# Optimization experiments

Hardware: AMD Instinct MI355X
Metric: run time of the kernel (lower is better)

The kernel has to match this reference:

```python
import jax, jax.numpy as jnp
import numpy as np

N, DEG, FIN, HID, OUT = 50000, 16, 128, 128, 64


def setup_inputs() -> dict:
    key = jax.random.key(0)
    ks = jax.random.split(key, 32)
    x = jax.random.normal(ks[0], (N, FIN), dtype=jnp.float32)
    src = jax.random.randint(ks[1], (N * DEG,), 0, N, dtype=jnp.int32)
    dst = jnp.repeat(jnp.arange(N, dtype=jnp.int32), DEG)  # sorted by target, fixed degree
    edge_index = jnp.stack([src, dst])  # [2, E]
    dims = [(FIN, HID), (HID, HID), (HID, OUT)]
    params = {}
    i = 2
    for l, (fi, fo) in enumerate(dims, 1):
        s_lstm = 1.0 / np.sqrt(fi)
        params[f"W_ih{l}"] = jax.random.normal(ks[i + 0], (4 * fi, fi)) * s_lstm
        params[f"W_hh{l}"] = jax.random.normal(ks[i + 1], (4 * fi, fi)) * s_lstm
        params[f"b_ih{l}"] = jax.random.normal(ks[i + 2], (4 * fi,)) * s_lstm
        params[f"b_hh{l}"] = jax.random.normal(ks[i + 3], (4 * fi,)) * s_lstm
        params[f"Wl{l}"] = jax.random.normal(ks[i + 4], (fo, fi)) * (1.0 / np.sqrt(fi))
        params[f"bl{l}"] = jnp.zeros((fo,), jnp.float32)
        params[f"Wr{l}"] = jax.random.normal(ks[i + 5], (fo, fi)) * (1.0 / np.sqrt(fi))
        i += 6
    return {"x": x, "edge_index": edge_index, **params}


def _lstm_last(neigh, Wih, Whh, bih, bhh):
    # neigh: [N, deg, Fi]; PyTorch LSTM gate order i,f,g,o; return last-step output h.
    h0 = jnp.zeros((neigh.shape[0], Wih.shape[0] // 4), neigh.dtype)
    bias = bih + bhh

    def step(carry, xt):
        h, c = carry
        g = xt @ Wih.T + h @ Whh.T + bias
        i, f, gg, o = jnp.split(g, 4, axis=-1)
        c = jax.nn.sigmoid(f) * c + jax.nn.sigmoid(i) * jnp.tanh(gg)
        h = jax.nn.sigmoid(o) * jnp.tanh(c)
        return (h, c), None

    (h, _), _ = jax.lax.scan(step, (h0, h0), jnp.swapaxes(neigh, 0, 1))
    return h


def _sage_layer(x, src2d, Wih, Whh, bih, bhh, Wl, bl, Wr):
    neigh = x[src2d]  # gather: [N, deg, Fi]
    aggr = _lstm_last(neigh, Wih, Whh, bih, bhh)  # [N, Fi]
    return aggr @ Wl.T + bl + x @ Wr.T  # lin_l(aggr) + lin_r(x)


def reference(x, edge_index,
              W_ih1, W_hh1, b_ih1, b_hh1, Wl1, bl1, Wr1,
              W_ih2, W_hh2, b_ih2, b_hh2, Wl2, bl2, Wr2,
              W_ih3, W_hh3, b_ih3, b_hh3, Wl3, bl3, Wr3):
    n = x.shape[0]
    src2d = edge_index[0].reshape(n, -1)  # fixed-degree, dst-sorted edge list
    h = _sage_layer(x, src2d, W_ih1, W_hh1, b_ih1, b_hh1, Wl1, bl1, Wr1)
    h = jax.nn.relu(h)  # dropout is identity in eval mode
    h = _sage_layer(h, src2d, W_ih2, W_hh2, b_ih2, b_hh2, Wl2, bl2, Wr2)
    h = jax.nn.relu(h)
    return _sage_layer(h, src2d, W_ih3, W_hh3, b_ih3, b_hh3, Wl3, bl3, Wr3)
```

## Files before the change

### kernel.cpp

```cpp
#include <hip/hip_runtime.h>
#include <cstddef>
#include <cstdint>

typedef __attribute__((ext_vector_type(4))) float f32x4;
typedef __attribute__((ext_vector_type(8))) short short8;

#define HID 128
#define NK1 -1.4426950408889634f
#define PK2 2.8853900817779268f

#define BAR_LGKM() __asm__ volatile("s_waitcnt lgkmcnt(0)\ns_barrier" ::: "memory")
#define STEP_BAR3() __asm__ volatile("s_waitcnt vmcnt(4) lgkmcnt(0)\ns_barrier" ::: "memory")

__device__ __forceinline__ short f2bf(float f) {
  unsigned u = __builtin_bit_cast(unsigned, f);
  u += 0x7FFFu + ((u >> 16) & 1u);
  return (short)(u >> 16);
}
__device__ __forceinline__ unsigned pack_bf2(float a, float b) {
  unsigned ua = __builtin_bit_cast(unsigned, a) + 0x8000u;
  unsigned ub = __builtin_bit_cast(unsigned, b) + 0x8000u;
  return __builtin_amdgcn_perm(ub, ua, 0x07060302u);
}
__device__ __forceinline__ float2 unpack2v(int w) {
  float2 r;
  r.x = __builtin_bit_cast(float, (unsigned)(w << 16));
  r.y = __builtin_bit_cast(float, (unsigned)w & 0xffff0000u);
  return r;
}

__device__ __forceinline__ float lstm_elem(float si, float sf, float sg, float so, float& c) {
  float Ei = __builtin_amdgcn_exp2f(si);
  float Ef = __builtin_amdgcn_exp2f(sf);
  float Tg = __builtin_amdgcn_exp2f(sg);
  float Eo = __builtin_amdgcn_exp2f(so);
  float u = 1.0f + Ei, w = 1.0f + Ef, v = Tg + 1.0f, Tm = Tg - 1.0f;
  float t0 = u * v;
  float num = __builtin_fmaf(c, t0, w * Tm);
  float cn = num * __builtin_amdgcn_rcpf(w * t0);
  c = cn;
  float Tc = __builtin_amdgcn_exp2f(PK2 * cn);
  return (Tc - 1.0f) * __builtin_amdgcn_rcpf((1.0f + Eo) * (Tc + 1.0f));
}

__global__ void conv_x_kernel(const float* __restrict__ x, short* __restrict__ xb, int n,
                              int* __restrict__ tctr) {
  int i = blockIdx.x * blockDim.x + threadIdx.x;
  if (i < 8) tctr[i] = 0;
  int stride = gridDim.x * blockDim.x;
  for (; i < n; i += stride) xb[i] = f2bf(x[i]);
}

__global__ void conv_layer_kernel(const float* __restrict__ Wih, const float* __restrict__ Whh,
                                  const float* __restrict__ bih, const float* __restrict__ bhh,
                                  const float* __restrict__ Wl, const float* __restrict__ Wr, int foK,
                                  short* __restrict__ wihB, short* __restrict__ whhB,
                                  short* __restrict__ wlB, short* __restrict__ wrB,
                                  float* __restrict__ bsum) {
  int i = blockIdx.x * blockDim.x + threadIdx.x;
  if (i < 512 * HID) {
    float sc = ((i >> 14) == 2) ? PK2 : NK1;
    wihB[i] = f2bf(Wih[i] * sc);
    whhB[i] = f2bf(Whh[i] * sc);
  }
  if (i < foK) { wlB[i] = f2bf(Wl[i]); wrB[i] = f2bf(Wr[i]); }
  if (i < 512) bsum[i] = (bih[i] + bhh[i]) * (((i >> 7) == 2) ? PK2 : NK1);
}

#define OSTR 524
__global__ __launch_bounds__(512, 4) void pgemm_kernel(
    const short* __restrict__ A, const short* __restrict__ W,
    const float* __restrict__ bias, short* __restrict__ out, int M, int ntiles) {
  __shared__ short ldsO[32 * OSTR];
  const int tid = threadIdx.x;
  const int wave = tid >> 6, lane = tid & 63;
  const int quad = lane >> 4, nn = lane & 15;
  const int cbase = wave * 64;

  short8 wreg[4][4];
#pragma unroll
  for (int kt = 0; kt < 4; ++kt)
#pragma unroll
    for (int nt = 0; nt < 4; ++nt)
      wreg[kt][nt] = *(const short8*)(W + (size_t)(cbase + nt * 16 + nn) * HID + kt * 32 + quad * 8);
  f32x4 bias4[4];
#pragma unroll
  for (int nt = 0; nt < 4; ++nt)
#pragma unroll
    for (int r = 0; r < 4; ++r) bias4[nt][r] = bias[cbase + nt * 16 + quad * 4 + r];

#pragma unroll 1
  for (int rt = blockIdx.x; rt < ntiles; rt += gridDim.x) {
    const int row0 = rt * 32;
    f32x4 acc[2][4];
#pragma unroll
    for (int b = 0; b < 2; ++b)
#pragma unroll
      for (int nt = 0; nt < 4; ++nt) acc[b][nt] = bias4[nt];
#pragma unroll
    for (int kt = 0; kt < 4; ++kt) {
      int r0 = row0 + nn;      if (r0 > M - 1) r0 = M - 1;
      int r1 = row0 + 16 + nn; if (r1 > M - 1) r1 = M - 1;
      short8 af0 = *(const short8*)(A + (size_t)r0 * HID + kt * 32 + quad * 8);
      short8 af1 = *(const short8*)(A + (size_t)r1 * HID + kt * 32 + quad * 8);
#pragma unroll
      for (int nt = 0; nt < 4; ++nt) {
        acc[0][nt] = __builtin_amdgcn_mfma_f32_16x16x32_bf16(wreg[kt][nt], af0, acc[0][nt], 0, 0, 0);
        acc[1][nt] = __builtin_amdgcn_mfma_f32_16x16x32_bf16(wreg[kt][nt], af1, acc[1][nt], 0, 0, 0);
      }
    }
    BAR_LGKM();
#pragma unroll
    for (int b = 0; b < 2; ++b)
#pragma unroll
      for (int nt = 0; nt < 4; ++nt) {
        uint2 pk;
        pk.x = pack_bf2(acc[b][nt][0], acc[b][nt][1]);
        pk.y = pack_bf2(acc[b][nt][2], acc[b][nt][3]);
        *(uint2*)(ldsO + (b * 16 + nn) * OSTR + cbase + nt * 16 + quad * 4) = pk;
      }
    BAR_LGKM();
#pragma unroll
    for (int idx = tid; idx < 32 * 64; idx += 512) {
      int row = idx >> 6, c8 = (idx & 63) * 8;
      if (row0 + row < M)
        *(short8*)(out + (size_t)(row0 + row) * 512 + c8) = *(const short8*)(ldsO + row * OSTR + c8);
    }
  }
}

#define NPB 16
#define PSTR 520
#define HSTR 152
#define LSTM_LDS_BYTES ((4 * NPB * PSTR + 2 * NPB * HSTR) * 2 + 256 * 4 + 16)

template <int FO, bool RELU, bool OUTF32>
__global__ __launch_bounds__(512, 4) void lstm_fused_kernel(
    const short* __restrict__ P, const short* __restrict__ Whh,
    const int* __restrict__ src, const short* __restrict__ cur,
    const short* __restrict__ Wl, const short* __restrict__ Wr,
    const float* __restrict__ bl,
    short* __restrict__ outB, float* __restrict__ outF, int M, int ntiles,
    int* __restrict__ tctr) {
  extern __shared__ char smem[];
  short* Pb = (short*)smem;
  short* Hb = Pb + 4 * NPB * PSTR;
  int* srcL = (int*)(Hb + 2 * NPB * HSTR);
  int* nextTp = srcL + 256;

  const int tid = threadIdx.x;
  const int wave = tid >> 6, lane = tid & 63;
  const int quad = lane >> 4, nn = lane & 15;
  const int r0row = wave * 2, r1row = wave * 2 + 1;

  short8 wreg[4][4];
#pragma unroll
  for (int kt = 0; kt < 4; ++kt)
#pragma unroll
    for (int q = 0; q < 4; ++q)
      wreg[kt][q] = *(const short8*)(Whh + (size_t)(q * 128 + wave * 16 + nn) * HID + kt * 32 + quad * 8);

  f32x4 biasO = {0.f, 0.f, 0.f, 0.f};
  short8 wlR[4], wrR[4];
  if (FO == 128 || wave < 4) {
#pragma unroll
    for (int r = 0; r < 4; ++r) biasO[r] = bl[wave * 16 + quad * 4 + r];
#pragma unroll
    for (int kt = 0; kt < 4; ++kt) {
      wlR[kt] = *(const short8*)(Wl + (size_t)(wave * 16 + nn) * HID + kt * 32 + quad * 8);
      wrR[kt] = *(const short8*)(Wr + (size_t)(wave * 16 + nn) * HID + kt * 32 + quad * 8);
    }
  }

  int tile = blockIdx.x;
  while (tile < ntiles) {
    const int nodeBase = tile * NPB;
    if (tid < 256) {
      int node = nodeBase + (tid >> 4);
      srcL[tid] = (node < M) ? src[nodeBase * 16 + tid] : 0;
    }
    if (tid == 0) *nextTp = (int)gridDim.x + atomicAdd(tctr, 1);
    float c_st[4] = {0.f, 0.f, 0.f, 0.f};
    BAR_LGKM();
    const int my_next = *nextTp;

#pragma unroll
    for (int tt = 0; tt < 3; ++tt) {
      int sa = srcL[r0row * 16 + tt], sb = srcL[r1row * 16 + tt];
      __builtin_amdgcn_global_load_lds(
          (const __attribute__((address_space(1))) unsigned int*)(P + (size_t)sa * 512 + lane * 8),
          (__attribute__((address_space(3))) unsigned int*)(Pb + tt * NPB * PSTR + r0row * PSTR), 16, 0, 0);
      __builtin_amdgcn_global_load_lds(
          (const __attribute__((address_space(1))) unsigned int*)(P + (size_t)sb * 512 + lane * 8),
          (__attribute__((address_space(3))) unsigned int*)(Pb + tt * NPB * PSTR + r1row * PSTR), 16, 0, 0);
    }
    int sA = srcL[r0row * 16 + 3], sB = srcL[r1row * 16 + 3];

    int pc = 0, pg = 3;
#pragma unroll 1
    for (int t = 0; t < 16; ++t) {
      short* Pc = Pb + pc * NPB * PSTR;
      short* Pg = Pb + pg * NPB * PSTR;
      const short* Hp = Hb + ((t + 1) & 1) * NPB * HSTR;
      short* Hw = Hb + (t & 1) * NPB * HSTR;
      pc = (pc + 1) & 3;
      pg = (pg + 1) & 3;

      STEP_BAR3();

      const short* pR = Pc + nn * PSTR + wave * 16 + quad * 4;
      uint2 p0 = *(const uint2*)(pR + 0 * 128);
      uint2 p1 = *(const uint2*)(pR + 1 * 128);
      uint2 p2 = *(const uint2*)(pR + 2 * 128);
      uint2 p3 = *(const uint2*)(pR + 3 * 128);
      f32x4 acc[4];
      {
        float2 u, v;
        u = unpack2v(p0.x); v = unpack2v(p0.y);
        acc[0][0] = u.x; acc[0][1] = u.y; acc[0][2] = v.x; acc[0][3] = v.y;
        u = unpack2v(p1.x); v = unpack2v(p1.y);
        acc[1][0] = u.x; acc[1][1] = u.y; acc[1][2] = v.x; acc[1][3] = v.y;
        u = unpack2v(p2.x); v = unpack2v(p2.y);
        acc[2][0] = u.x; acc[2][1] = u.y; acc[2][2] = v.x; acc[2][3] = v.y;
        u = unpack2v(p3.x); v = unpack2v(p3.y);
        acc[3][0] = u.x; acc[3][1] = u.y; acc[3][2] = v.x; acc[3][3] = v.y;
      }

      __builtin_amdgcn_global_load_lds(
          (const __attribute__((address_space(1))) unsigned int*)(P + (size_t)sA * 512 + lane * 8),
          (__attribute__((address_space(3))) unsigned int*)(Pg + r0row * PSTR), 16, 0, 0);
      __builtin_amdgcn_global_load_lds(
          (const __attribute__((address_space(1))) unsigned int*)(P + (size_t)sB * 512 + lane * 8),
          (__attribute__((address_space(3))) unsigned int*)(Pg + r1row * PSTR), 16, 0, 0);
      {
        int tn = (t + 4 < 16) ? t + 4 : 15;
        sA = srcL[r0row * 16 + tn];
        sB = srcL[r1row * 16 + tn];
      }

      if (t) {
#pragma unroll
        for (int kt = 0; kt < 4; ++kt) {
          short8 hb = *(const short8*)(Hp + nn * HSTR + kt * 32 + quad * 8);
#pragma unroll
          for (int q = 0; q < 4; ++q)
            acc[q] = __builtin_amdgcn_mfma_f32_16x16x32_bf16(wreg[kt][q], hb, acc[q], 0, 0, 0);
        }
      }

      float hv[4];
#pragma unroll
      for (int r = 0; r < 4; ++r)
        hv[r] = lstm_elem(acc[0][r], acc[1][r], acc[2][r], acc[3][r], c_st[r]);
      uint2 pk;
      pk.x = pack_bf2(hv[0], hv[1]);
      pk.y = pack_bf2(hv[2], hv[3]);
      *(uint2*)(Hw + nn * HSTR + wave * 16 + quad * 4) = pk;
    }

    BAR_LGKM();

    if (FO == 128 || wave < 4) {
      const short* Hf = Hb + NPB * HSTR;
      const int cbase = wave * 16;
      f32x4 accO = biasO;
#pragma unroll
      for (int kt = 0; kt < 4; ++kt) {
        short8 hb = *(const short8*)(Hf + nn * HSTR + kt * 32 + quad * 8);
        accO = __builtin_amdgcn_mfma_f32_16x16x32_bf16(wlR[kt], hb, accO, 0, 0, 0);
        short8 cb = *(const short8*)(cur + (size_t)(nodeBase + nn) * HID + kt * 32 + quad * 8);
        accO = __builtin_amdgcn_mfma_f32_16x16x32_bf16(wrR[kt], cb, accO, 0, 0, 0);
      }
      if (RELU) {
#pragma unroll
        for (int r = 0; r < 4; ++r) accO[r] = fmaxf(accO[r], 0.0f);
      }
      int node = nodeBase + nn;
      if (node < M) {
        if (OUTF32) {
          *(f32x4*)(outF + (size_t)node * FO + cbase + quad * 4) = accO;
        } else {
          uint2 pko;
          pko.x = pack_bf2(accO[0], accO[1]);
          pko.y = pack_bf2(accO[2], accO[3]);
          *(uint2*)(outB + (size_t)node * FO + cbase + quad * 4) = pko;
        }
      }
    }
    tile = my_next;
  }
}

extern "C" void kernel_launch(void* const* d_in, const int* in_sizes, int n_in,
                              void* d_out, int out_size, void* d_ws, size_t ws_size,
                              hipStream_t stream) {
  const float* x = (const float*)d_in[0];
  const int* src = (const int*)d_in[1];
  const float* Wih[3] = {(const float*)d_in[2], (const float*)d_in[9], (const float*)d_in[16]};
  const float* Whh[3] = {(const float*)d_in[3], (const float*)d_in[10], (const float*)d_in[17]};
  const float* bih[3] = {(const float*)d_in[4], (const float*)d_in[11], (const float*)d_in[18]};
  const float* bhh[3] = {(const float*)d_in[5], (const float*)d_in[12], (const float*)d_in[19]};
  const float* Wl[3]  = {(const float*)d_in[6], (const float*)d_in[13], (const float*)d_in[20]};
  const float* bl[3]  = {(const float*)d_in[7], (const float*)d_in[14], (const float*)d_in[21]};
  const float* Wr[3]  = {(const float*)d_in[8], (const float*)d_in[15], (const float*)d_in[22]};

  const int M = in_sizes[0] / HID;

  char* ws = (char*)d_ws;
  size_t off = 0;
  auto alloc = [&](size_t bytes) -> void* {
    void* p = ws + off;
    off += (bytes + 255) & ~(size_t)255;
    return p;
  };
  short* curA = (short*)alloc((size_t)M * HID * 2);
  short* curB = (short*)alloc((size_t)M * HID * 2);
  short* Pbuf = (short*)alloc((size_t)M * 512 * 2);
  short* wihB[3]; short* whhB[3]; short* wlB[3]; short* wrB[3]; float* bsum[3];
  for (int l = 0; l < 3; ++l) {
    wihB[l] = (short*)alloc(512 * HID * 2);
    whhB[l] = (short*)alloc(512 * HID * 2);
    wlB[l]  = (short*)alloc(HID * HID * 2);
    wrB[l]  = (short*)alloc(HID * HID * 2);
    bsum[l] = (float*)alloc(512 * 4);
  }
  int* tctr = (int*)alloc(256);

  const int nltiles = (M + NPB - 1) / NPB;
  const int ntiles = (M + 31) / 32;

  (void)hipFuncSetAttribute((const void*)lstm_fused_kernel<128, true, false>,
                            hipFuncAttributeMaxDynamicSharedMemorySize, LSTM_LDS_BYTES);
  (void)hipFuncSetAttribute((const void*)lstm_fused_kernel<64, false, true>,
                            hipFuncAttributeMaxDynamicSharedMemorySize, LSTM_LDS_BYTES);

  conv_x_kernel<<<2048, 256, 0, stream>>>(x, curA, M * HID, tctr);
  for (int l = 0; l < 3; ++l) {
    const int Fo = (l == 2) ? 64 : 128;
    conv_layer_kernel<<<256, 256, 0, stream>>>(Wih[l], Whh[l], bih[l], bhh[l], Wl[l], Wr[l],
                                               Fo * HID, wihB[l], whhB[l], wlB[l], wrB[l], bsum[l]);
  }

  short* cur = curA;
  short* nxt = curB;
  for (int l = 0; l < 3; ++l) {
    pgemm_kernel<<<784, 512, 0, stream>>>(cur, wihB[l], bsum[l], Pbuf, M, ntiles);
    if (l < 2) {
      lstm_fused_kernel<128, true, false><<<512, 512, LSTM_LDS_BYTES, stream>>>(
          Pbuf, whhB[l], src, cur, wlB[l], wrB[l], bl[l], nxt, nullptr, M, nltiles, tctr + l);
      short* tswap = cur; cur = nxt; nxt = tswap;
    } else {
      lstm_fused_kernel<64, false, true><<<512, 512, LSTM_LDS_BYTES, stream>>>(
          Pbuf, whhB[l], src, cur, wlB[l], wrB[l], bl[l], nullptr, (float*)d_out, M, nltiles, tctr + 2);
    }
  }
}
```

Measured before the change: 787.2 us.

## Process 32 nodes per LSTM tile with triple-buffered neighbor prefetch

Doubles the node tile of the fused LSTM kernel from 16 to 32, so each wave issues two MFMA chains against the same register-resident W_hh fragments. That gives more independent work per weight load and per barrier. The P prefetch ring shrinks from four buffers to three, which shortens the lookahead from three steps to two. Launch bounds and grid size are halved to match. The larger LDS footprint likely limits residency to one block per CU. The epilogue is rebalanced so that all eight waves take part in the 64-wide output layer.

```diff
diff --git a/kernel.cpp b/kernel.cpp
--- a/kernel.cpp
+++ b/kernel.cpp
@@ -10,7 +10,7 @@
 #define PK2 2.8853900817779268f
 
 #define BAR_LGKM() __asm__ volatile("s_waitcnt lgkmcnt(0)\ns_barrier" ::: "memory")
-#define STEP_BAR3() __asm__ volatile("s_waitcnt vmcnt(4) lgkmcnt(0)\ns_barrier" ::: "memory")
+#define STEP_BAR() __asm__ volatile("s_waitcnt vmcnt(4) lgkmcnt(0)\ns_barrier" ::: "memory")
 
 __device__ __forceinline__ short f2bf(float f) {
   unsigned u = __builtin_bit_cast(unsigned, f);
@@ -129,13 +129,14 @@
   }
 }
 
-#define NPB 16
+#define NPB 32
 #define PSTR 520
 #define HSTR 152
-#define LSTM_LDS_BYTES ((4 * NPB * PSTR + 2 * NPB * HSTR) * 2 + 256 * 4 + 16)
+#define NPBUF 3
+#define LSTM_LDS_BYTES ((NPBUF * NPB * PSTR + 2 * NPB * HSTR) * 2 + 512 * 4 + 16)
 
 template <int FO, bool RELU, bool OUTF32>
-__global__ __launch_bounds__(512, 4) void lstm_fused_kernel(
+__global__ __launch_bounds__(512, 2) void lstm_fused_kernel(
     const short* __restrict__ P, const short* __restrict__ Whh,
     const int* __restrict__ src, const short* __restrict__ cur,
     const short* __restrict__ Wl, const short* __restrict__ Wr,
@@ -144,14 +145,14 @@
     int* __restrict__ tctr) {
   extern __shared__ char smem[];
   short* Pb = (short*)smem;
-  short* Hb = Pb + 4 * NPB * PSTR;
+  short* Hb = Pb + NPBUF * NPB * PSTR;
   int* srcL = (int*)(Hb + 2 * NPB * HSTR);
-  int* nextTp = srcL + 256;
+  int* nextTp = srcL + 512;
 
   const int tid = threadIdx.x;
   const int wave = tid >> 6, lane = tid & 63;
   const int quad = lane >> 4, nn = lane & 15;
-  const int r0row = wave * 2, r1row = wave * 2 + 1;
+  const int grow = wave * 4;
 
   short8 wreg[4][4];
 #pragma unroll
@@ -160,131 +161,178 @@
     for (int q = 0; q < 4; ++q)
       wreg[kt][q] = *(const short8*)(Whh + (size_t)(q * 128 + wave * 16 + nn) * HID + kt * 32 + quad * 8);
 
-  f32x4 biasO = {0.f, 0.f, 0.f, 0.f};
+  const int ecol = (FO == 128) ? wave * 16 : (wave & 3) * 16;
+  f32x4 biasO;
   short8 wlR[4], wrR[4];
-  if (FO == 128 || wave < 4) {
-#pragma unroll
-    for (int r = 0; r < 4; ++r) biasO[r] = bl[wave * 16 + quad * 4 + r];
-#pragma unroll
-    for (int kt = 0; kt < 4; ++kt) {
-      wlR[kt] = *(const short8*)(Wl + (size_t)(wave * 16 + nn) * HID + kt * 32 + quad * 8);
-      wrR[kt] = *(const short8*)(Wr + (size_t)(wave * 16 + nn) * HID + kt * 32 + quad * 8);
-    }
+#pragma unroll
+  for (int r = 0; r < 4; ++r) biasO[r] = bl[ecol + quad * 4 + r];
+#pragma unroll
+  for (int kt = 0; kt < 4; ++kt) {
+    wlR[kt] = *(const short8*)(Wl + (size_t)(ecol + nn) * HID + kt * 32 + quad * 8);
+    wrR[kt] = *(const short8*)(Wr + (size_t)(ecol + nn) * HID + kt * 32 + quad * 8);
   }
 
   int tile = blockIdx.x;
   while (tile < ntiles) {
     const int nodeBase = tile * NPB;
-    if (tid < 256) {
+    {
       int node = nodeBase + (tid >> 4);
       srcL[tid] = (node < M) ? src[nodeBase * 16 + tid] : 0;
     }
     if (tid == 0) *nextTp = (int)gridDim.x + atomicAdd(tctr, 1);
-    float c_st[4] = {0.f, 0.f, 0.f, 0.f};
+    float c0[4] = {0.f, 0.f, 0.f, 0.f};
+    float c1[4] = {0.f, 0.f, 0.f, 0.f};
     BAR_LGKM();
     const int my_next = *nextTp;
 
 #pragma unroll
-    for (int tt = 0; tt < 3; ++tt) {
-      int sa = srcL[r0row * 16 + tt], sb = srcL[r1row * 16 + tt];
-      __builtin_amdgcn_global_load_lds(
-          (const __attribute__((address_space(1))) unsigned int*)(P + (size_t)sa * 512 + lane * 8),
-          (__attribute__((address_space(3))) unsigned int*)(Pb + tt * NPB * PSTR + r0row * PSTR), 16, 0, 0);
-      __builtin_amdgcn_global_load_lds(
-          (const __attribute__((address_space(1))) unsigned int*)(P + (size_t)sb * 512 + lane * 8),
-          (__attribute__((address_space(3))) unsigned int*)(Pb + tt * NPB * PSTR + r1row * PSTR), 16, 0, 0);
-    }
-    int sA = srcL[r0row * 16 + 3], sB = srcL[r1row * 16 + 3];
-
-    int pc = 0, pg = 3;
+    for (int tt = 0; tt < 2; ++tt) {
+#pragma unroll
+      for (int j = 0; j < 4; ++j) {
+        int s = srcL[(grow + j) * 16 + tt];
+        __builtin_amdgcn_global_load_lds(
+            (const __attribute__((address_space(1))) unsigned int*)(P + (size_t)s * 512 + lane * 8),
+            (__attribute__((address_space(3))) unsigned int*)(Pb + tt * NPB * PSTR + (grow + j) * PSTR),
+            16, 0, 0);
+      }
+    }
+
+    int pc = 0, pg = 2;
 #pragma unroll 1
     for (int t = 0; t < 16; ++t) {
       short* Pc = Pb + pc * NPB * PSTR;
       short* Pg = Pb + pg * NPB * PSTR;
       const short* Hp = Hb + ((t + 1) & 1) * NPB * HSTR;
       short* Hw = Hb + (t & 1) * NPB * HSTR;
-      pc = (pc + 1) & 3;
-      pg = (pg + 1) & 3;
-
-      STEP_BAR3();
-
-      const short* pR = Pc + nn * PSTR + wave * 16 + quad * 4;
-      uint2 p0 = *(const uint2*)(pR + 0 * 128);
-      uint2 p1 = *(const uint2*)(pR + 1 * 128);
-      uint2 p2 = *(const uint2*)(pR + 2 * 128);
-      uint2 p3 = *(const uint2*)(pR + 3 * 128);
-      f32x4 acc[4];
+      pc = (pc == NPBUF - 1) ? 0 : pc + 1;
+      pg = (pg == NPBUF - 1) ? 0 : pg + 1;
+
+      STEP_BAR();
+
+      f32x4 acc0[4], acc1[4];
       {
+        const short* pR = Pc + nn * PSTR + wave * 16 + quad * 4;
+        uint2 q0 = *(const uint2*)(pR + 0 * 128);
+        uint2 q1 = *(const uint2*)(pR + 1 * 128);
+        uint2 q2 = *(const uint2*)(pR + 2 * 128);
+        uint2 q3 = *(const uint2*)(pR + 3 * 128);
         float2 u, v;
-        u = unpack2v(p0.x); v = unpack2v(p0.y);
-        acc[0][0] = u.x; acc[0][1] = u.y; acc[0][2] = v.x; acc[0][3] = v.y;
-        u = unpack2v(p1.x); v = unpack2v(p1.y);
-        acc[1][0] = u.x; acc[1][1] = u.y; acc[1][2] = v.x; acc[1][3] = v.y;
-        u = unpack2v(p2.x); v = unpack2v(p2.y);
-        acc[2][0] = u.x; acc[2][1] = u.y; acc[2][2] = v.x; acc[2][3] = v.y;
-        u = unpack2v(p3.x); v = unpack2v(p3.y);
-        acc[3][0] = u.x; acc[3][1] = u.y; acc[3][2] = v.x; acc[3][3] = v.y;
-      }
-
-      __builtin_amdgcn_global_load_lds(
-          (const __attribute__((address_space(1))) unsigned int*)(P + (size_t)sA * 512 + lane * 8),
-          (__attribute__((address_space(3))) unsigned int*)(Pg + r0row * PSTR), 16, 0, 0);
-      __builtin_amdgcn_global_load_lds(
-          (const __attribute__((address_space(1))) unsigned int*)(P + (size_t)sB * 512 + lane * 8),
-          (__attribute__((address_space(3))) unsigned int*)(Pg + r1row * PSTR), 16, 0, 0);
+        u = unpack2v(q0.x); v = unpack2v(q0.y);
+        acc0[0][0] = u.x; acc0[0][1] = u.y; acc0[0][2] = v.x; acc0[0][3] = v.y;
+        u = unpack2v(q1.x); v = unpack2v(q1.y);
+        acc0[1][0] = u.x; acc0[1][1] = u.y; acc0[1][2] = v.x; acc0[1][3] = v.y;
+        u = unpack2v(q2.x); v = unpack2v(q2.y);
+        acc0[2][0] = u.x; acc0[2][1] = u.y; acc0[2][2] = v.x; acc0[2][3] = v.y;
+        u = unpack2v(q3.x); v = unpack2v(q3.y);
+        acc0[3][0] = u.x; acc0[3][1] = u.y; acc0[3][2] = v.x; acc0[3][3] = v.y;
+      }
       {
-        int tn = (t + 4 < 16) ? t + 4 : 15;
-        sA = srcL[r0row * 16 + tn];
-        sB = srcL[r1row * 16 + tn];
+        const short* pR = Pc + (16 + nn) * PSTR + wave * 16 + quad * 4;
+        uint2 q0 = *(const uint2*)(pR + 0 * 128);
+        uint2 q1 = *(const uint2*)(pR + 1 * 128);
+        uint2 q2 = *(const uint2*)(pR + 2 * 128);
+        uint2 q3 = *(const uint2*)(pR + 3 * 128);
+        float2 u, v;
+        u = unpack2v(q0.x); v = unpack2v(q0.y);
+        acc1[0][0] = u.x; acc1[0][1] = u.y; acc1[0][2] = v.x; acc1[0][3] = v.y;
+        u = unpack2v(q1.x); v = unpack2v(q1.y);
+        acc1[1][0] = u.x; acc1[1][1] = u.y; acc1[1][2] = v.x; acc1[1][3] = v.y;
+        u = unpack2v(q2.x); v = unpack2v(q2.y);
+        acc1[2][0] = u.x; acc1[2][1] = u.y; acc1[2][2] = v.x; acc1[2][3] = v.y;
+        u = unpack2v(q3.x); v = unpack2v(q3.y);
+        acc1[3][0] = u.x; acc1[3][1] = u.y; acc1[3][2] = v.x; acc1[3][3] = v.y;
+      }
+
+      {
+        int tn = (t + 2 < 16) ? t + 2 : 15;
+#pragma unroll
+        for (int j = 0; j < 4; ++j) {
+          int s = srcL[(grow + j) * 16 + tn];
+          __builtin_amdgcn_global_load_lds(
+              (const __attribute__((address_space(1))) unsigned int*)(P + (size_t)s * 512 + lane * 8),
+              (__attribute__((address_space(3))) unsigned int*)(Pg + (grow + j) * PSTR), 16, 0, 0);
+        }
       }
 
       if (t) {
 #pragma unroll
         for (int kt = 0; kt < 4; ++kt) {
-          short8 hb = *(const short8*)(Hp + nn * HSTR + kt * 32 + quad * 8);
-#pragma unroll
-          for (int q = 0; q < 4; ++q)
-            acc[q] = __builtin_amdgcn_mfma_f32_16x16x32_bf16(wreg[kt][q], hb, acc[q], 0, 0, 0);
-        }
-      }
-
-      float hv[4];
+          short8 hb0 = *(const short8*)(Hp + nn * HSTR + kt * 32 + quad * 8);
+          short8 hb1 = *(const short8*)(Hp + (16 + nn) * HSTR + kt * 32 + quad * 8);
+#pragma unroll
+          for (int q = 0; q < 4; ++q) {
+            acc0[q] = __builtin_amdgcn_mfma_f32_16x16x32_bf16(wreg[kt][q], hb0, acc0[q], 0, 0, 0);
+            acc1[q] = __builtin_amdgcn_mfma_f32_16x16x32_bf16(wreg[kt][q], hb1, acc1[q], 0, 0, 0);
+          }
+        }
+      }
+
+      float hv0[4], hv1[4];
 #pragma unroll
       for (int r = 0; r < 4; ++r)
-        hv[r] = lstm_elem(acc[0][r], acc[1][r], acc[2][r], acc[3][r], c_st[r]);
-      uint2 pk;
-      pk.x = pack_bf2(hv[0], hv[1]);
-      pk.y = pack_bf2(hv[2], hv[3]);
-      *(uint2*)(Hw + nn * HSTR + wave * 16 + quad * 4) = pk;
+        hv0[r] = lstm_elem(acc0[0][r], acc0[1][r], acc0[2][r], acc0[3][r], c0[r]);
+#pragma unroll
+      for (int r = 0; r < 4; ++r)
+        hv1[r] = lstm_elem(acc1[0][r], acc1[1][r], acc1[2][r], acc1[3][r], c1[r]);
+      uint2 pk0, pk1;
+      pk0.x = pack_bf2(hv0[0], hv0[1]);
+      pk0.y = pack_bf2(hv0[2], hv0[3]);
+      pk1.x = pack_bf2(hv1[0], hv1[1]);
+      pk1.y = pack_bf2(hv1[2], hv1[3]);
+      *(uint2*)(Hw + nn * HSTR + wave * 16 + quad * 4) = pk0;
+      *(uint2*)(Hw + (16 + nn) * HSTR + wave * 16 + quad * 4) = pk1;
     }
 
     BAR_LGKM();
 
-    if (FO == 128 || wave < 4) {
+    {
       const short* Hf = Hb + NPB * HSTR;
-      const int cbase = wave * 16;
-      f32x4 accO = biasO;
-#pragma unroll
-      for (int kt = 0; kt < 4; ++kt) {
-        short8 hb = *(const short8*)(Hf + nn * HSTR + kt * 32 + quad * 8);
-        accO = __builtin_amdgcn_mfma_f32_16x16x32_bf16(wlR[kt], hb, accO, 0, 0, 0);
-        short8 cb = *(const short8*)(cur + (size_t)(nodeBase + nn) * HID + kt * 32 + quad * 8);
-        accO = __builtin_amdgcn_mfma_f32_16x16x32_bf16(wrR[kt], cb, accO, 0, 0, 0);
-      }
-      if (RELU) {
-#pragma unroll
-        for (int r = 0; r < 4; ++r) accO[r] = fmaxf(accO[r], 0.0f);
-      }
-      int node = nodeBase + nn;
-      if (node < M) {
-        if (OUTF32) {
-          *(f32x4*)(outF + (size_t)node * FO + cbase + quad * 4) = accO;
-        } else {
+      if (FO == 128) {
+        f32x4 accO0 = biasO, accO1 = biasO;
+#pragma unroll
+        for (int kt = 0; kt < 4; ++kt) {
+          short8 hb0 = *(const short8*)(Hf + nn * HSTR + kt * 32 + quad * 8);
+          short8 hb1 = *(const short8*)(Hf + (16 + nn) * HSTR + kt * 32 + quad * 8);
+          accO0 = __builtin_amdgcn_mfma_f32_16x16x32_bf16(wlR[kt], hb0, accO0, 0, 0, 0);
+          accO1 = __builtin_amdgcn_mfma_f32_16x16x32_bf16(wlR[kt], hb1, accO1, 0, 0, 0);
+          short8 cb0 = *(const short8*)(cur + (size_t)(nodeBase + nn) * HID + kt * 32 + quad * 8);
+          short8 cb1 = *(const short8*)(cur + (size_t)(nodeBase + 16 + nn) * HID + kt * 32 + quad * 8);
+          accO0 = __builtin_amdgcn_mfma_f32_16x16x32_bf16(wrR[kt], cb0, accO0, 0, 0, 0);
+          accO1 = __builtin_amdgcn_mfma_f32_16x16x32_bf16(wrR[kt], cb1, accO1, 0, 0, 0);
+        }
+        if (RELU) {
+#pragma unroll
+          for (int r = 0; r < 4; ++r) {
+            accO0[r] = fmaxf(accO0[r], 0.0f);
+            accO1[r] = fmaxf(accO1[r], 0.0f);
+          }
+        }
+        int node0 = nodeBase + nn, node1 = nodeBase + 16 + nn;
+        if (node0 < M) {
           uint2 pko;
-          pko.x = pack_bf2(accO[0], accO[1]);
-          pko.y = pack_bf2(accO[2], accO[3]);
-          *(uint2*)(outB + (size_t)node * FO + cbase + quad * 4) = pko;
-        }
+          pko.x = pack_bf2(accO0[0], accO0[1]);
+          pko.y = pack_bf2(accO0[2], accO0[3]);
+          *(uint2*)(outB + (size_t)node0 * FO + ecol + quad * 4) = pko;
+        }
+        if (node1 < M) {
+          uint2 pko;
+          pko.x = pack_bf2(accO1[0], accO1[1]);
+          pko.y = pack_bf2(accO1[2], accO1[3]);
+          *(uint2*)(outB + (size_t)node1 * FO + ecol + quad * 4) = pko;
+        }
+      } else {
+        const int half = wave >> 2;
+        f32x4 accO = biasO;
+#pragma unroll
+        for (int kt = 0; kt < 4; ++kt) {
+          short8 hb = *(const short8*)(Hf + (half * 16 + nn) * HSTR + kt * 32 + quad * 8);
+          accO = __builtin_amdgcn_mfma_f32_16x16x32_bf16(wlR[kt], hb, accO, 0, 0, 0);
+          short8 cb = *(const short8*)(cur + (size_t)(nodeBase + half * 16 + nn) * HID + kt * 32 + quad * 8);
+          accO = __builtin_amdgcn_mfma_f32_16x16x32_bf16(wrR[kt], cb, accO, 0, 0, 0);
+        }
+        int node = nodeBase + half * 16 + nn;
+        if (node < M)
+          *(f32x4*)(outF + (size_t)node * FO + ecol + quad * 4) = accO;
       }
     }
     tile = my_next;
@@ -346,11 +394,11 @@
   for (int l = 0; l < 3; ++l) {
     pgemm_kernel<<<784, 512, 0, stream>>>(cur, wihB[l], bsum[l], Pbuf, M, ntiles);
     if (l < 2) {
-      lstm_fused_kernel<128, true, false><<<512, 512, LSTM_LDS_BYTES, stream>>>(
+      lstm_fused_kernel<128, true, false><<<256, 512, LSTM_LDS_BYTES, stream>>>(
           Pbuf, whhB[l], src, cur, wlB[l], wrB[l], bl[l], nxt, nullptr, M, nltiles, tctr + l);
       short* tswap = cur; cur = nxt; nxt = tswap;
     } else {
-      lstm_fused_kernel<64, false, true><<<512, 512, LSTM_LDS_BYTES, stream>>>(
+      lstm_fused_kernel<64, false, true><<<256, 512, LSTM_LDS_BYTES, stream>>>(
           Pbuf, whhB[l], src, cur, wlB[l], wrB[l], bl[l], nullptr, (float*)d_out, M, nltiles, tctr + 2);
     }
   }
```

Measured after the change: 908.5 us. 1.15x slower.
